# Kernel tuning notes

Hardware: AMD Instinct MI355X
Metric: run time of the kernel (lower is better)

## Reference

```python
import jax, jax.numpy as jnp
import numpy as np

B, L, I, H, C, E = 32, 2048, 512, 512, 512, 512
TEMP = 0.5
EPS = 1e-20


def setup_inputs() -> dict:
    key = jax.random.key(0)
    ks = jax.random.split(key, 8)
    s_in = 1.0 / np.sqrt(I)
    s_h = 1.0 / np.sqrt(H)
    s_c = 1.0 / np.sqrt(C)
    return {
        "inputs_BxLxI": jax.random.normal(ks[0], (B, L, I), dtype=jnp.float32),
        "W_h": jax.random.uniform(ks[1], (H, I), jnp.float32, -s_in, s_in),
        "b_h": jax.random.uniform(ks[2], (H,), jnp.float32, -s_in, s_in),
        "W_logits": jax.random.uniform(ks[3], (C, H), jnp.float32, -s_h, s_h),
        "b_logits": jax.random.uniform(ks[4], (C,), jnp.float32, -s_h, s_h),
        "codebook_CxE": jax.random.uniform(ks[5], (C, E), jnp.float32, -s_c, s_c),
        "u_noise": jax.random.uniform(ks[6], (B, L, C), dtype=jnp.float32),
        "testing": 0,
    }


def reference(inputs_BxLxI, W_h, b_h, W_logits, b_logits, codebook_CxE, u_noise, testing):
    # 1-layer MLP before quantization
    hiddens = jax.nn.relu(jnp.einsum('bli,hi->blh', inputs_BxLxI, W_h) + b_h)
    logits_BxLxC = jnp.einsum('blh,ch->blc', hiddens, W_logits) + b_logits

    if testing:
        ind = jnp.argmax(logits_BxLxC, axis=-1)
        onehot_BxLxC = jax.nn.one_hot(ind, C, dtype=logits_BxLxC.dtype)
    else:
        # gumbel-softmax with straight-through one-hot
        g = -jnp.log(-jnp.log(u_noise + EPS) + EPS)
        y = jax.nn.softmax((logits_BxLxC + g) / TEMP, axis=-1)
        ind = jnp.argmax(y, axis=-1)
        y_hard = jax.nn.one_hot(ind, C, dtype=y.dtype)
        onehot_BxLxC = jax.lax.stop_gradient(y_hard - y) + y

    # disguised embedding gather: onehot @ codebook
    codes_BxLxE = jnp.einsum('blc,ce->ble', onehot_BxLxC, codebook_CxE)
    return (logits_BxLxC, codes_BxLxE)
```

## Files before the change

### kernel.cpp

```cpp
#include <hip/hip_runtime.h>
#include <hip/hip_fp16.h>

typedef _Float16 h16;
typedef __attribute__((ext_vector_type(8))) _Float16 h16x8;
typedef __attribute__((ext_vector_type(4))) _Float16 h16x4;
typedef __attribute__((ext_vector_type(4))) float f32x4;

#define KDIM 512
#define NDIM 512
#define LO_SCALE 4096.0f
#define LO_INV   0.000244140625f

__device__ __forceinline__ void gload16(const void* g, void* l) {
  __builtin_amdgcn_global_load_lds((const __attribute__((address_space(1))) void*)g,
                                   (__attribute__((address_space(3))) void*)l, 16, 0, 0);
}

#define WAITV(n) asm volatile("s_waitcnt vmcnt(" #n ")" ::: "memory")
#define WAITL0() asm volatile("s_waitcnt lgkmcnt(0)" ::: "memory")
#define SB() __builtin_amdgcn_sched_barrier(0)

__global__ void split_w(const float* __restrict__ Wh, const float* __restrict__ Wl,
                        h16* __restrict__ WhHi, h16* __restrict__ WhLo,
                        h16* __restrict__ WlHi, h16* __restrict__ WlLo) {
  int i = blockIdx.x * 256 + threadIdx.x;
  float a = Wh[i];
  h16 h = (h16)a;
  WhHi[i] = h; WhLo[i] = (h16)((a - (float)h) * LO_SCALE);
  a = Wl[i];
  h = (h16)a;
  WlHi[i] = h; WlLo[i] = (h16)((a - (float)h) * LO_SCALE);
}

__launch_bounds__(256, 2)
__global__ void gemm7_k(const float* __restrict__ X,
                        const h16* __restrict__ BHi, const h16* __restrict__ BLo,
                        const float* __restrict__ bias,
                        h16* __restrict__ OHi, h16* __restrict__ OLo) {
  __shared__ __align__(16) char lds[81920];
  const int tid = threadIdx.x;
  const int wave = tid >> 6, lane = tid & 63;
  const int wn = wave;
  const int wg = (blockIdx.x & 7) * 256 + (blockIdx.x >> 3);
  const int bm = wg >> 1, bn = wg & 1;
  const long arow0 = (long)bm * 64;
  const int brow0 = bn * 256;
  const int q = lane >> 4, rlo = lane & 15;

  f32x4 acc_hh[4][4] = {};
  f32x4 acc_mx[4][4] = {};
  f32x4 areg[2][2];

  const int axrow = tid >> 2;
  const int akb = (tid & 3) * 32;
  const int ajb = (tid & 3) * 16;
  const int asw = ((axrow & 1) << 6) | (((axrow >> 1) & 3) << 4);

  auto aload = [&](f32x4 (&ar)[2], int kt) {
    const char* base = (const char*)X + (arow0 + axrow) * 2048 + (long)kt * 128 + akb;
    ar[0] = *(const f32x4*)base;
    ar[1] = *(const f32x4*)(base + 16);
  };
  auto awrite = [&](const f32x4 (&ar)[2], char* buf) {
    h16x8 hv, lv;
#pragma unroll
    for (int p = 0; p < 2; ++p)
#pragma unroll
      for (int e = 0; e < 4; ++e) {
        float a = ar[p][e];
        h16 h = (h16)a;
        hv[p * 4 + e] = h;
        lv[p * 4 + e] = (h16)((a - (float)h) * LO_SCALE);
      }
    *(h16x8*)(buf + axrow * 128 + (ajb ^ asw)) = hv;
    *(h16x8*)(buf + axrow * 128 + ((ajb + 64) ^ asw)) = lv;
  };
  auto bgld = [&](char* buf, int kt) {
#pragma unroll
    for (int pass = 0; pass < 8; ++pass) {
      int p = pass * 4096 + tid * 16;
      int row = p >> 7;
      int gs = ((p >> 4) & 7) ^ (row & 7);
      const char* sp = (gs & 4) ? (const char*)BLo : (const char*)BHi;
      long off = (long)(brow0 + row) * 1024 + (long)kt * 64 + (gs & 3) * 16;
      gload16(sp + off, buf + 8192 + pass * 4096 + wave * 1024);
    }
  };

  aload(areg[0], 0);
  aload(areg[1], 1);
  WAITV(2);
  awrite(areg[0], lds);
  bgld(lds, 0);
  WAITV(8);
  awrite(areg[1], lds + 40960);
  aload(areg[0], 2);
  bgld(lds + 40960, 1);
  WAITL0();

#pragma unroll
  for (int t = 0; t < 16; ++t) {
    if (t <= 13) { WAITV(10); } else if (t == 14) { WAITV(8); } else { WAITV(0); }
    SB();
    __builtin_amdgcn_s_barrier();
    SB();

    if (t <= 12) aload(areg[(t + 3) & 1], t + 3);

    char* buf = lds + (t & 1) * 40960;
    h16x8 ah[4], al[4], bh[4], bl[4];
#pragma unroll
    for (int i = 0; i < 4; ++i) {
      int row = i * 16 + rlo;
      int swa = ((row & 1) << 6) | (((row >> 1) & 3) << 4);
      ah[i] = *(const h16x8*)(buf + row * 128 + ((q * 16) ^ swa));
      al[i] = *(const h16x8*)(buf + row * 128 + ((q * 16 + 64) ^ swa));
      int rb = wn * 64 + i * 16 + rlo;
      int swb = (rb & 7) << 4;
      bh[i] = *(const h16x8*)(buf + 8192 + rb * 128 + ((q * 16) ^ swb));
      bl[i] = *(const h16x8*)(buf + 8192 + rb * 128 + ((q * 16 + 64) ^ swb));
    }
#pragma unroll
    for (int i = 0; i < 4; ++i)
#pragma unroll
      for (int j = 0; j < 4; ++j)
        acc_hh[i][j] = __builtin_amdgcn_mfma_f32_16x16x32_f16(ah[i], bh[j], acc_hh[i][j], 0, 0, 0);
#pragma unroll
    for (int i = 0; i < 4; ++i)
#pragma unroll
      for (int j = 0; j < 4; ++j)
        acc_mx[i][j] = __builtin_amdgcn_mfma_f32_16x16x32_f16(ah[i], bl[j], acc_mx[i][j], 0, 0, 0);
#pragma unroll
    for (int i = 0; i < 4; ++i)
#pragma unroll
      for (int j = 0; j < 4; ++j)
        acc_mx[i][j] = __builtin_amdgcn_mfma_f32_16x16x32_f16(al[i], bh[j], acc_mx[i][j], 0, 0, 0);

    WAITL0();
    SB();
    __builtin_amdgcn_s_barrier();
    SB();
    if (t <= 12) {
      WAITV(10);
      awrite(areg[(t + 2) & 1], lds + (t & 1) * 40960);
      bgld(lds + (t & 1) * 40960, t + 2);
    } else if (t == 13) {
      WAITV(8);
      awrite(areg[1], lds + 40960);
      bgld(lds + 40960, 15);
    }
  }

#pragma unroll
  for (int j = 0; j < 4; ++j) {
    int lcol = wn * 64 + j * 16 + rlo;
    float bv = bias[bn * 256 + lcol];
#pragma unroll
    for (int i = 0; i < 4; ++i)
#pragma unroll
      for (int r = 0; r < 4; ++r) {
        int lrow = i * 16 + q * 4 + r;
        float v = fmaxf(acc_hh[i][j][r] + acc_mx[i][j][r] * LO_INV + bv, 0.0f);
        h16 h = (h16)v;
        h16 l = (h16)((v - (float)h) * LO_SCALE);
        unsigned uu = (unsigned)__builtin_bit_cast(unsigned short, h) |
                      ((unsigned)__builtin_bit_cast(unsigned short, l) << 16);
        *(unsigned*)(lds + lrow * 1024 + lcol * 4) = uu;
      }
  }
  __syncthreads();
#pragma unroll
  for (int pass = 0; pass < 16; ++pass) {
    int o = pass * 4096 + tid * 16;
    int lrow = o >> 10;
    int lcb = o & 1023;
    uint4 d = *(const uint4*)(lds + o);
    uint2 hi, lo;
    hi.x = (d.x & 0xffffu) | (d.y << 16);
    hi.y = (d.z & 0xffffu) | (d.w << 16);
    lo.x = (d.x >> 16) | (d.y & 0xffff0000u);
    lo.y = (d.z >> 16) | (d.w & 0xffff0000u);
    long gb = (arow0 + lrow) * 1024 + bn * 512 + (lcb >> 1);
    *(uint2*)((char*)OHi + gb) = hi;
    *(uint2*)((char*)OLo + gb) = lo;
  }
}

template <int EPI>
__launch_bounds__(256, 2)
__global__ void gemm4_k(const h16* __restrict__ AHi, const h16* __restrict__ ALo,
                        const h16* __restrict__ BHi, const h16* __restrict__ BLo,
                        const float* __restrict__ bias,
                        float* __restrict__ Cf32,
                        h16* __restrict__ OHi, h16* __restrict__ OLo) {
  __shared__ __align__(16) char lds[65536];
  const int tid = threadIdx.x;
  const int wave = tid >> 6, lane = tid & 63;
  const int wg = (blockIdx.x & 7) * 256 + (blockIdx.x >> 3);
  const int bm = wg >> 2, bn = wg & 3;
  const int wm = wave >> 1, wn = wave & 1;
  const long arow0 = (long)bm * 128;
  const int brow0 = bn * 128;
  const int q = lane >> 4, rlo = lane & 15;

  f32x4 acc_hh[4][4] = {};
  f32x4 acc_mx[4][4] = {};

#define STAGE4(bufoff, kt)                                                    \
  {                                                                           \
    _Pragma("unroll")                                                         \
    for (int pass = 0; pass < 4; ++pass) {                                    \
      int p = pass * 4096 + wave * 1024 + lane * 16;                          \
      int row = p >> 7;                                                       \
      int gs = ((p >> 4) & 7) ^ (row & 7);                                    \
      const char* sp = (gs & 4) ? (const char*)ALo : (const char*)AHi;        \
      long off = (arow0 + row) * 1024 + (kt) * 64 + (gs & 3) * 16;            \
      gload16(sp + off, lds + (bufoff) + pass * 4096 + wave * 1024);          \
    }                                                                         \
    _Pragma("unroll")                                                         \
    for (int pass = 0; pass < 4; ++pass) {                                    \
      int p = pass * 4096 + wave * 1024 + lane * 16;                          \
      int row = p >> 7;                                                       \
      int gs = ((p >> 4) & 7) ^ (row & 7);                                    \
      const char* sp = (gs & 4) ? (const char*)BLo : (const char*)BHi;        \
      long off = (long)(brow0 + row) * 1024 + (kt) * 64 + (gs & 3) * 16;      \
      gload16(sp + off, lds + (bufoff) + 16384 + pass * 4096 + wave * 1024);  \
    }                                                                         \
  }

  STAGE4(0, 0);
  STAGE4(32768, 1);

#pragma unroll
  for (int t = 0; t < 16; ++t) {
    if (t < 15) { WAITV(8); } else { WAITV(0); }
    SB();
    __builtin_amdgcn_s_barrier();
    SB();

    const char* buf = lds + (t & 1) * 32768;
    h16x8 ah[4], al[4], bh[4], bl[4];
#pragma unroll
    for (int i = 0; i < 4; ++i) {
      int row = wm * 64 + i * 16 + rlo;
      int sw = (row & 7) << 4;
      ah[i] = *(const h16x8*)(buf + row * 128 + ((q * 16) ^ sw));
      al[i] = *(const h16x8*)(buf + row * 128 + ((q * 16 + 64) ^ sw));
      int rb = wn * 64 + i * 16 + rlo;
      int swb = (rb & 7) << 4;
      bh[i] = *(const h16x8*)(buf + 16384 + rb * 128 + ((q * 16) ^ swb));
      bl[i] = *(const h16x8*)(buf + 16384 + rb * 128 + ((q * 16 + 64) ^ swb));
    }
#pragma unroll
    for (int i = 0; i < 4; ++i)
#pragma unroll
      for (int j = 0; j < 4; ++j)
        acc_hh[i][j] = __builtin_amdgcn_mfma_f32_16x16x32_f16(ah[i], bh[j], acc_hh[i][j], 0, 0, 0);
#pragma unroll
    for (int i = 0; i < 4; ++i)
#pragma unroll
      for (int j = 0; j < 4; ++j)
        acc_mx[i][j] = __builtin_amdgcn_mfma_f32_16x16x32_f16(ah[i], bl[j], acc_mx[i][j], 0, 0, 0);
#pragma unroll
    for (int i = 0; i < 4; ++i)
#pragma unroll
      for (int j = 0; j < 4; ++j)
        acc_mx[i][j] = __builtin_amdgcn_mfma_f32_16x16x32_f16(al[i], bh[j], acc_mx[i][j], 0, 0, 0);

    WAITL0();
    SB();
    __builtin_amdgcn_s_barrier();
    SB();
    if (t + 2 < 16) STAGE4((t & 1) * 32768, t + 2);
  }
#undef STAGE4

#pragma unroll
  for (int j = 0; j < 4; ++j) {
    int lcol = wn * 64 + j * 16 + rlo;
    float bv = bias[bn * 128 + lcol];
#pragma unroll
    for (int i = 0; i < 4; ++i)
#pragma unroll
      for (int r = 0; r < 4; ++r) {
        int lrow = wm * 64 + i * 16 + q * 4 + r;
        float v = acc_hh[i][j][r] + acc_mx[i][j][r] * LO_INV + bv;
        if (EPI == 0) {
          v = fmaxf(v, 0.0f);
          h16 h = (h16)v;
          h16 l = (h16)((v - (float)h) * LO_SCALE);
          unsigned uu = (unsigned)__builtin_bit_cast(unsigned short, h) |
                        ((unsigned)__builtin_bit_cast(unsigned short, l) << 16);
          *(unsigned*)(lds + lrow * 512 + lcol * 4) = uu;
        } else {
          *(float*)(lds + lrow * 512 + lcol * 4) = v;
        }
      }
  }
  __syncthreads();
#pragma unroll
  for (int pass = 0; pass < 16; ++pass) {
    int o = pass * 4096 + tid * 16;
    int lrow = o >> 9;
    int lcb = o & 511;
    if (EPI == 0) {
      uint4 d = *(const uint4*)(lds + o);
      uint2 hi, lo;
      hi.x = (d.x & 0xffffu) | (d.y << 16);
      hi.y = (d.z & 0xffffu) | (d.w << 16);
      lo.x = (d.x >> 16) | (d.y & 0xffff0000u);
      lo.y = (d.z >> 16) | (d.w & 0xffff0000u);
      long gb = (arow0 + lrow) * 1024 + bn * 256 + (lcb >> 1);
      *(uint2*)((char*)OHi + gb) = hi;
      *(uint2*)((char*)OLo + gb) = lo;
    } else {
      f32x4 d = *(const f32x4*)(lds + o);
      long gb = (arow0 + lrow) * 2048 + bn * 512 + lcb;
      *(f32x4*)((char*)Cf32 + gb) = d;
    }
  }
}

__global__ void k3_argmax_gather(const float* __restrict__ logits,
                                 const float* __restrict__ u,
                                 const float* __restrict__ cb,
                                 const int* __restrict__ testing,
                                 float* __restrict__ codes) {
  const int wave = threadIdx.x >> 6, lane = threadIdx.x & 63;
  const long row = (long)blockIdx.x * 4 + wave;
  const f32x4* lrow = (const f32x4*)(logits + row * 512);
  const f32x4* urow = (const f32x4*)(u + row * 512);
  const int test = *testing;

  float best = -3.4e38f;
  int bi = 0;
#pragma unroll
  for (int h = 0; h < 2; ++h) {
    int c4 = h * 64 + lane;
    f32x4 z = lrow[c4];
    if (!test) {
      f32x4 uu = urow[c4];
#pragma unroll
      for (int t = 0; t < 4; ++t)
        z[t] += -logf(-logf(uu[t] + 1e-20f) + 1e-20f);
    }
#pragma unroll
    for (int t = 0; t < 4; ++t) {
      int c = c4 * 4 + t;
      if (z[t] > best) { best = z[t]; bi = c; }
    }
  }
#pragma unroll
  for (int off = 32; off; off >>= 1) {
    float ob = __shfl_xor(best, off);
    int oi = __shfl_xor(bi, off);
    if (ob > best || (ob == best && oi < bi)) { best = ob; bi = oi; }
  }
  const f32x4* src = (const f32x4*)(cb + (long)bi * 512);
  f32x4* dst = (f32x4*)(codes + row * 512);
  dst[lane] = src[lane];
  dst[lane + 64] = src[lane + 64];
}

extern "C" void kernel_launch(void* const* d_in, const int* in_sizes, int n_in,
                              void* d_out, int out_size, void* d_ws, size_t ws_size,
                              hipStream_t stream) {
  const float* X = (const float*)d_in[0];
  const float* Wh = (const float*)d_in[1];
  const float* bh = (const float*)d_in[2];
  const float* Wl = (const float*)d_in[3];
  const float* bl = (const float*)d_in[4];
  const float* cb = (const float*)d_in[5];
  const float* u = (const float*)d_in[6];
  const int* testing = (const int*)d_in[7];

  float* logits = (float*)d_out;
  float* codes = logits + 33554432;
  h16* Hhi = (h16*)codes;
  h16* Hlo = Hhi + 33554432;

  h16* WhHi = (h16*)d_ws;
  h16* WhLo = WhHi + 262144;
  h16* WlHi = WhLo + 262144;
  h16* WlLo = WlHi + 262144;

  split_w<<<dim3(1024), dim3(256), 0, stream>>>(Wh, Wl, WhHi, WhLo, WlHi, WlLo);

  gemm7_k<<<dim3(2048), dim3(256), 0, stream>>>(X, WhHi, WhLo, bh, Hhi, Hlo);

  gemm4_k<1><<<dim3(2048), dim3(256), 0, stream>>>(Hhi, Hlo, WlHi, WlLo, bl,
                                                   logits, nullptr, nullptr);

  k3_argmax_gather<<<dim3(16384), dim3(256), 0, stream>>>(logits, u, cb, testing, codes);
}
```

Baseline: 311.6 us.

## Retile first GEMM to 128x128 with 8 waves and 4-stage LDS pipeline

The first (input-projection) GEMM now runs with 512 threads per block. The output tile changes from 64x256 to 128x128, split over a 2x4 wave grid. The LDS ring grows from two stages to four, so there is one barrier per k-step instead of two. The next stage's A conversion and B global-to-LDS loads are issued between the hi*hi and cross-term MFMA groups, and s_setprio raises wave priority around the MFMAs. The aim is better operand reuse and overlap of memory with matrix math. The cost is 128KB of LDS per block, which limits occupancy to one large block per CU, and tighter WAITV(0) waits.

```diff
diff --git a/kernel.cpp b/kernel.cpp
--- a/kernel.cpp
+++ b/kernel.cpp
@@ -32,23 +32,23 @@
   WlHi[i] = h; WlLo[i] = (h16)((a - (float)h) * LO_SCALE);
 }
 
-__launch_bounds__(256, 2)
-__global__ void gemm7_k(const float* __restrict__ X,
+__launch_bounds__(512, 2)
+__global__ void gemm8_k(const float* __restrict__ X,
                         const h16* __restrict__ BHi, const h16* __restrict__ BLo,
                         const float* __restrict__ bias,
                         h16* __restrict__ OHi, h16* __restrict__ OLo) {
-  __shared__ __align__(16) char lds[81920];
+  __shared__ __align__(16) char lds[131072];
   const int tid = threadIdx.x;
   const int wave = tid >> 6, lane = tid & 63;
-  const int wn = wave;
+  const int wm = wave >> 2, wn = wave & 3;
   const int wg = (blockIdx.x & 7) * 256 + (blockIdx.x >> 3);
-  const int bm = wg >> 1, bn = wg & 1;
-  const long arow0 = (long)bm * 64;
-  const int brow0 = bn * 256;
+  const int bm = wg >> 2, bn = wg & 3;
+  const long arow0 = (long)bm * 128;
+  const int brow0 = bn * 128;
   const int q = lane >> 4, rlo = lane & 15;
 
-  f32x4 acc_hh[4][4] = {};
-  f32x4 acc_mx[4][4] = {};
+  f32x4 acc_hh[4][2] = {};
+  f32x4 acc_mx[4][2] = {};
   f32x4 areg[2][2];
 
   const int axrow = tid >> 2;
@@ -77,13 +77,26 @@
   };
   auto bgld = [&](char* buf, int kt) {
 #pragma unroll
-    for (int pass = 0; pass < 8; ++pass) {
-      int p = pass * 4096 + tid * 16;
+    for (int pass = 0; pass < 2; ++pass) {
+      int p = pass * 8192 + tid * 16;
       int row = p >> 7;
       int gs = ((p >> 4) & 7) ^ (row & 7);
       const char* sp = (gs & 4) ? (const char*)BLo : (const char*)BHi;
       long off = (long)(brow0 + row) * 1024 + (long)kt * 64 + (gs & 3) * 16;
-      gload16(sp + off, buf + 8192 + pass * 4096 + wave * 1024);
+      gload16(sp + off, buf + 16384 + pass * 8192 + (tid >> 6) * 1024 +
+                        (tid & 63) * 0);
+    }
+  };
+
+  auto bgld2 = [&](char* buf, int kt) {
+#pragma unroll
+    for (int pass = 0; pass < 2; ++pass) {
+      int p = pass * 8192 + wave * 1024 + lane * 16;
+      int row = p >> 7;
+      int gs = ((p >> 4) & 7) ^ (row & 7);
+      const char* sp = (gs & 4) ? (const char*)BLo : (const char*)BHi;
+      long off = (long)(brow0 + row) * 1024 + (long)kt * 64 + (gs & 3) * 16;
+      gload16(sp + off, buf + 16384 + pass * 8192 + wave * 1024);
     }
   };
 
@@ -91,96 +104,104 @@
   aload(areg[1], 1);
   WAITV(2);
   awrite(areg[0], lds);
-  bgld(lds, 0);
-  WAITV(8);
-  awrite(areg[1], lds + 40960);
+  bgld2(lds, 0);
   aload(areg[0], 2);
-  bgld(lds + 40960, 1);
+  WAITV(2);
+  awrite(areg[1], lds + 32768);
+  bgld2(lds + 32768, 1);
+  aload(areg[1], 3);
+  WAITV(2);
+  awrite(areg[0], lds + 65536);
+  bgld2(lds + 65536, 2);
+  aload(areg[0], 4);
   WAITL0();
+  SB();
 
 #pragma unroll
   for (int t = 0; t < 16; ++t) {
-    if (t <= 13) { WAITV(10); } else if (t == 14) { WAITV(8); } else { WAITV(0); }
-    SB();
     __builtin_amdgcn_s_barrier();
     SB();
 
-    if (t <= 12) aload(areg[(t + 3) & 1], t + 3);
-
-    char* buf = lds + (t & 1) * 40960;
-    h16x8 ah[4], al[4], bh[4], bl[4];
+    char* buf = lds + (t & 3) * 32768;
+    h16x8 ah[4], al[4], bh[2], bl[2];
 #pragma unroll
     for (int i = 0; i < 4; ++i) {
-      int row = i * 16 + rlo;
+      int row = wm * 64 + i * 16 + rlo;
       int swa = ((row & 1) << 6) | (((row >> 1) & 3) << 4);
       ah[i] = *(const h16x8*)(buf + row * 128 + ((q * 16) ^ swa));
       al[i] = *(const h16x8*)(buf + row * 128 + ((q * 16 + 64) ^ swa));
-      int rb = wn * 64 + i * 16 + rlo;
+    }
+#pragma unroll
+    for (int j = 0; j < 2; ++j) {
+      int rb = wn * 32 + j * 16 + rlo;
       int swb = (rb & 7) << 4;
-      bh[i] = *(const h16x8*)(buf + 8192 + rb * 128 + ((q * 16) ^ swb));
-      bl[i] = *(const h16x8*)(buf + 8192 + rb * 128 + ((q * 16 + 64) ^ swb));
-    }
-#pragma unroll
-    for (int i = 0; i < 4; ++i)
-#pragma unroll
-      for (int j = 0; j < 4; ++j)
+      bh[j] = *(const h16x8*)(buf + 16384 + rb * 128 + ((q * 16) ^ swb));
+      bl[j] = *(const h16x8*)(buf + 16384 + rb * 128 + ((q * 16 + 64) ^ swb));
+    }
+
+    __builtin_amdgcn_s_setprio(1);
+#pragma unroll
+    for (int i = 0; i < 4; ++i)
+#pragma unroll
+      for (int j = 0; j < 2; ++j)
         acc_hh[i][j] = __builtin_amdgcn_mfma_f32_16x16x32_f16(ah[i], bh[j], acc_hh[i][j], 0, 0, 0);
-#pragma unroll
-    for (int i = 0; i < 4; ++i)
-#pragma unroll
-      for (int j = 0; j < 4; ++j)
+    __builtin_amdgcn_s_setprio(0);
+
+    if (t <= 12) {
+      WAITV(0);
+      awrite(areg[(t + 3) & 1], lds + ((t + 3) & 3) * 32768);
+      bgld2(lds + ((t + 3) & 3) * 32768, t + 3);
+      if (t <= 11) aload(areg[(t + 4) & 1], t + 4);
+    }
+
+    __builtin_amdgcn_s_setprio(1);
+#pragma unroll
+    for (int i = 0; i < 4; ++i)
+#pragma unroll
+      for (int j = 0; j < 2; ++j)
         acc_mx[i][j] = __builtin_amdgcn_mfma_f32_16x16x32_f16(ah[i], bl[j], acc_mx[i][j], 0, 0, 0);
 #pragma unroll
     for (int i = 0; i < 4; ++i)
 #pragma unroll
-      for (int j = 0; j < 4; ++j)
+      for (int j = 0; j < 2; ++j)
         acc_mx[i][j] = __builtin_amdgcn_mfma_f32_16x16x32_f16(al[i], bh[j], acc_mx[i][j], 0, 0, 0);
+    __builtin_amdgcn_s_setprio(0);
 
     WAITL0();
     SB();
-    __builtin_amdgcn_s_barrier();
-    SB();
-    if (t <= 12) {
-      WAITV(10);
-      awrite(areg[(t + 2) & 1], lds + (t & 1) * 40960);
-      bgld(lds + (t & 1) * 40960, t + 2);
-    } else if (t == 13) {
-      WAITV(8);
-      awrite(areg[1], lds + 40960);
-      bgld(lds + 40960, 15);
-    }
-  }
-
-#pragma unroll
-  for (int j = 0; j < 4; ++j) {
-    int lcol = wn * 64 + j * 16 + rlo;
-    float bv = bias[bn * 256 + lcol];
+  }
+
+  __builtin_amdgcn_s_barrier();
+#pragma unroll
+  for (int j = 0; j < 2; ++j) {
+    int lcol = wn * 32 + j * 16 + rlo;
+    float bv = bias[bn * 128 + lcol];
 #pragma unroll
     for (int i = 0; i < 4; ++i)
 #pragma unroll
       for (int r = 0; r < 4; ++r) {
-        int lrow = i * 16 + q * 4 + r;
+        int lrow = wm * 64 + i * 16 + q * 4 + r;
         float v = fmaxf(acc_hh[i][j][r] + acc_mx[i][j][r] * LO_INV + bv, 0.0f);
         h16 h = (h16)v;
         h16 l = (h16)((v - (float)h) * LO_SCALE);
         unsigned uu = (unsigned)__builtin_bit_cast(unsigned short, h) |
                       ((unsigned)__builtin_bit_cast(unsigned short, l) << 16);
-        *(unsigned*)(lds + lrow * 1024 + lcol * 4) = uu;
+        *(unsigned*)(lds + lrow * 512 + lcol * 4) = uu;
       }
   }
   __syncthreads();
 #pragma unroll
-  for (int pass = 0; pass < 16; ++pass) {
-    int o = pass * 4096 + tid * 16;
-    int lrow = o >> 10;
-    int lcb = o & 1023;
+  for (int pass = 0; pass < 8; ++pass) {
+    int o = pass * 8192 + tid * 16;
+    int lrow = o >> 9;
+    int lcb = o & 511;
     uint4 d = *(const uint4*)(lds + o);
     uint2 hi, lo;
     hi.x = (d.x & 0xffffu) | (d.y << 16);
     hi.y = (d.z & 0xffffu) | (d.w << 16);
     lo.x = (d.x >> 16) | (d.y & 0xffff0000u);
     lo.y = (d.z >> 16) | (d.w & 0xffff0000u);
-    long gb = (arow0 + lrow) * 1024 + bn * 512 + (lcb >> 1);
+    long gb = (arow0 + lrow) * 1024 + bn * 256 + (lcb >> 1);
     *(uint2*)((char*)OHi + gb) = hi;
     *(uint2*)((char*)OLo + gb) = lo;
   }
@@ -386,7 +407,7 @@
 
   split_w<<<dim3(1024), dim3(256), 0, stream>>>(Wh, Wl, WhHi, WhLo, WlHi, WlLo);
 
-  gemm7_k<<<dim3(2048), dim3(256), 0, stream>>>(X, WhHi, WhLo, bh, Hhi, Hlo);
+  gemm8_k<<<dim3(2048), dim3(512), 0, stream>>>(X, WhHi, WhLo, bh, Hhi, Hlo);
 
   gemm4_k<1><<<dim3(2048), dim3(256), 0, stream>>>(Hhi, Hlo, WlHi, WlLo, bl,
                                                    logits, nullptr, nullptr);
```

Result: slower. 331.8 us (+6.5%).
